# Kernel optimization log

Hardware: AMD Instinct MI355X
Metric: run time of the kernel (lower is better)

## Reference

```python
import jax, jax.numpy as jnp
import numpy as np

B = 128          # batch of codewords
M_CHK = 288      # n_check_nodes
N_VAR = 576      # n_variable_nodes
K_INFO = 288     # n_information_bits
N_ITER = 5
EDGE_P = 0.02    # ~11-12 edges per check row, LDPC-like sparsity


def setup_inputs() -> dict:
    key = jax.random.key(0)
    k1, k2, k3, k4 = jax.random.split(key, 4)
    inputs = jax.random.normal(k1, (B, N_VAR), dtype=jnp.float32)
    # sparse binary parity-check matrix, batched (keras RNN constants carry batch dim)
    H = jax.random.bernoulli(k2, EDGE_P, (B, M_CHK, N_VAR)).astype(jnp.float32)
    sigma2 = 0.5 + 0.5 * jax.random.uniform(k3, (B, 1), dtype=jnp.float32)
    # learned parameters
    input_ponderation = jnp.ones((N_ITER, 1), dtype=jnp.float32)
    out_ponderation = jnp.ones((N_ITER, 1), dtype=jnp.float32)
    skip_ponderation = jnp.ones((1, 1), dtype=jnp.float32)
    # per-edge check-to-variable weights of the neural BP cell
    w_cv = 1.0 + 0.02 * jax.random.normal(k4, (M_CHK, N_VAR), dtype=jnp.float32)
    gate_logit = jnp.asarray(0.0, dtype=jnp.float32)
    return {"inputs": inputs, "H": H, "sigma2": sigma2,
            "input_ponderation": input_ponderation,
            "out_ponderation": out_ponderation,
            "skip_ponderation": skip_ponderation,
            "w_cv": w_cv, "gate_logit": gate_logit}


def _decode(inputs, H, sigma2, input_ponderation, out_ponderation,
            skip_ponderation, w_cv, gate_logit):
    llrs = -4.0 * inputs / sigma2                                    # [B, n]
    # trainable=True path: normalize by mean |llr|
    norm_llrs = llrs / jnp.mean(jnp.abs(llrs), axis=-1, keepdims=True)
    # tile over iterations and apply input ponderation -> [B, T, n]
    x = norm_llrs[:, None, :] * input_ponderation

    mask = H                                                         # [B, m, n]
    gate = jax.nn.sigmoid(gate_logit)

    def cell(Mstate, x_t):
        # variable-to-check extrinsic messages on edges
        S = jnp.sum(Mstate, axis=1, keepdims=True)                   # [B, 1, n]
        V = (x_t[:, None, :] + S - Mstate) * mask                    # [B, m, n]
        # tanh-product check-node update (product excluding self via divide)
        t = jnp.tanh(0.5 * jnp.clip(V, -15.0, 15.0))
        t_edge = jnp.where(mask > 0, t, 1.0)
        P = jnp.prod(t_edge, axis=-1, keepdims=True)                 # [B, m, 1]
        t_safe = jnp.where(jnp.abs(t_edge) < 1e-7,
                           jnp.where(t_edge >= 0, 1e-7, -1e-7), t_edge)
        r = jnp.clip(P / t_safe, -1.0 + 1e-6, 1.0 - 1e-6)
        M_new = 2.0 * jnp.arctanh(r) * w_cv * mask                   # weighted c2v
        # gated (damped) state update
        M_out = gate * M_new + (1.0 - gate) * Mstate
        posterior = x_t + jnp.sum(M_out, axis=1)                     # [B, n]
        return M_out, posterior

    M0 = jnp.zeros_like(H)
    xs = jnp.swapaxes(x, 0, 1)                                       # [T, B, n]
    _, posts = jax.lax.scan(cell, M0, xs)
    outputs = jnp.swapaxes(posts, 0, 1)                              # [B, T, n]

    # post-normalization per iteration, weighted pooling over iterations
    norm_out = outputs / jnp.mean(jnp.abs(outputs), axis=-1, keepdims=True)
    pooled = jnp.mean(out_ponderation * norm_out, axis=-2)           # [B, n]
    out = pooled + skip_ponderation * norm_llrs                      # [1,1] broadcast
    return jax.nn.sigmoid(-out[:, :K_INFO])


def reference(inputs, H, sigma2, input_ponderation, out_ponderation,
              skip_ponderation, w_cv, gate_logit):
    return _decode(inputs, H, sigma2, input_ponderation, out_ponderation,
                   skip_ponderation, w_cv, gate_logit)
```

## Files before the change

### kernel.cpp

```cpp
#include <hip/hip_runtime.h>

#define B_SZ 128
#define MCHK 288
#define NVAR 576
#define KINFO 288
#define NITER 5
#define CAP 40
#define LCAP 3712
#define TPB 1024
#define EPT 4

__device__ __align__(16) unsigned short g_idx[(size_t)B_SZ * MCHK * CAP];
__device__ int g_cnt[B_SZ * MCHK];

__global__ __launch_bounds__(256) void build_edges(const float* __restrict__ H) {
    const int row  = blockIdx.x * 4 + (threadIdx.x >> 6);
    const int lane = threadIdx.x & 63;
    const float* hrow = H + (size_t)row * NVAR;
    const float4* h4  = (const float4*)hrow;
    float4 a  = h4[lane];
    float4 bq = h4[64 + lane];
    float  c  = hrow[512 + lane];
    int cnt = (a.x!=0.f)+(a.y!=0.f)+(a.z!=0.f)+(a.w!=0.f)
            + (bq.x!=0.f)+(bq.y!=0.f)+(bq.z!=0.f)+(bq.w!=0.f) + (c!=0.f);
    int pre = cnt;
    #pragma unroll
    for (int o = 1; o < 64; o <<= 1) {
        int n = __shfl_up(pre, o, 64);
        if (lane >= o) pre += n;
    }
    int p = pre - cnt;
    unsigned short* dst = g_idx + (size_t)row * CAP;
    int base = lane * 4;
    if (a.x!=0.f)  { if (p<CAP) dst[p] = (unsigned short)(base    ); p++; }
    if (a.y!=0.f)  { if (p<CAP) dst[p] = (unsigned short)(base + 1); p++; }
    if (a.z!=0.f)  { if (p<CAP) dst[p] = (unsigned short)(base + 2); p++; }
    if (a.w!=0.f)  { if (p<CAP) dst[p] = (unsigned short)(base + 3); p++; }
    if (bq.x!=0.f) { if (p<CAP) dst[p] = (unsigned short)(256 + base    ); p++; }
    if (bq.y!=0.f) { if (p<CAP) dst[p] = (unsigned short)(256 + base + 1); p++; }
    if (bq.z!=0.f) { if (p<CAP) dst[p] = (unsigned short)(256 + base + 2); p++; }
    if (bq.w!=0.f) { if (p<CAP) dst[p] = (unsigned short)(256 + base + 3); p++; }
    if (c!=0.f)    { if (p<CAP) dst[p] = (unsigned short)(512 + lane);     p++; }
    if (lane == 63) g_cnt[row] = (pre > CAP) ? CAP : pre;
}

__global__ __launch_bounds__(TPB) void decode(
    const float* __restrict__ inp,   const float* __restrict__ sigma2,
    const float* __restrict__ ipond, const float* __restrict__ opond,
    const float* __restrict__ skipp, const float* __restrict__ wcv,
    const float* __restrict__ gatel, float* __restrict__ out) {

    __shared__ __align__(16) float MT[(MCHK * CAP) / 2];
    __shared__ unsigned int ev[LCAP];
    __shared__ float xln[NVAR];
    __shared__ float S[NVAR];
    __shared__ float Prow[MCHK];
    __shared__ int   rcnt[MCHK];
    __shared__ int   roff[MCHK];
    __shared__ float red[16];
    __shared__ float redT[NITER][16];
    __shared__ int   wsumI[16];
    __shared__ int   EtotS;

    float* const tld = MT;
    unsigned short* const stage = (unsigned short*)MT;

    const int b    = blockIdx.x;
    const int tid  = threadIdx.x;
    const int wid  = tid >> 6;
    const int lane = tid & 63;

    const float sig  = sigma2[b];
    const float gate = 1.0f / (1.0f + __expf(-gatel[0]));
    const float gbar = 1.0f - gate;
    const float skip = skipp[0];

    float ipl[NITER], opl[NITER];
    #pragma unroll
    for (int t = 0; t < NITER; ++t) { ipl[t] = ipond[t]; opl[t] = opond[t]; }

    float l = 0.0f;
    if (tid < NVAR) l = -4.0f * inp[(size_t)b * NVAR + tid] / sig;
    float al = (tid < NVAR) ? fabsf(l) : 0.0f;
    #pragma unroll
    for (int o = 32; o; o >>= 1) al += __shfl_down(al, o, 64);
    if (lane == 0) red[wid] = al;

    if (tid < MCHK) rcnt[tid] = g_cnt[b * MCHK + tid];
    {
        const uint4* src = (const uint4*)(g_idx + (size_t)b * (MCHK * CAP));
        uint4* dst = (uint4*)stage;
        const int n16 = (MCHK * CAP * 2) / 16;
        #pragma unroll
        for (int i = 0; i < 2; ++i) {
            const int j = tid + i * TPB;
            if (j < n16) dst[j] = src[j];
        }
    }
    __syncthreads();

    int myc = 0, incl = 0;
    if (tid < 320) {
        myc  = (tid < MCHK) ? rcnt[tid] : 0;
        incl = myc;
        #pragma unroll
        for (int o = 1; o < 64; o <<= 1) {
            int n = __shfl_up(incl, o, 64);
            if (lane >= o) incl += n;
        }
        if (lane == 63) wsumI[wid] = incl;
    }
    __syncthreads();
    if (tid < MCHK) {
        int o = incl - myc;
        #pragma unroll
        for (int w = 0; w < 4; ++w) if (w < wid) o += wsumI[w];
        int c = myc;
        if (o >= LCAP)         { o = 0; c = 0; }
        else if (o + c > LCAP) { c = LCAP - o; }
        roff[tid] = o; rcnt[tid] = c;
        const unsigned short* sg = stage + tid * CAP;
        for (int j = 0; j < c; ++j)
            ev[o + j] = ((unsigned)tid << 16) | (unsigned)sg[j];
    }
    if (tid < NVAR) S[tid] = 0.0f;
    if (tid == 0) {
        int e = wsumI[0] + wsumI[1] + wsumI[2] + wsumI[3] + wsumI[4];
        EtotS = (e > LCAP) ? LCAP : e;
    }
    __syncthreads();
    const int E = EtotS;

    {
        float s = 0.0f;
        #pragma unroll
        for (int i = 0; i < 16; ++i) s += red[i];
        const float sc = (float)NVAR / s;
        if (tid < NVAR) xln[tid] = l * sc;
    }
    unsigned evr[EPT]; float wre[EPT], Ml[EPT], tre[EPT];
    #pragma unroll
    for (int k = 0; k < EPT; ++k) {
        evr[k] = 0u; wre[k] = 0.0f; Ml[k] = 0.0f; tre[k] = 0.0f;
        const int e = tid + k * TPB;
        if (e < E) {
            const unsigned pk = ev[e];
            evr[k] = pk;
            wre[k] = wcv[(pk >> 16) * NVAR + (pk & 0xFFFFu)];
        }
    }
    __syncthreads();

    float p[NITER];
    #pragma unroll
    for (int t = 0; t < NITER; ++t) { p[t] = 0.0f; }

    #pragma unroll
    for (int t = 0; t < NITER; ++t) {
        const float pt = ipl[t];

        #pragma unroll
        for (int k = 0; k < EPT; ++k) {
            const int e = tid + k * TPB;
            if (e < E) {
                const int v = (int)(evr[k] & 0xFFFFu);
                float V = fmaf(pt, xln[v], S[v]) - Ml[k];
                V = fminf(15.0f, fmaxf(-15.0f, V));
                float ex = __expf(V);
                float te = (ex - 1.0f) * __builtin_amdgcn_rcpf(ex + 1.0f);
                float x  = 0.5f * V, x2 = x * x;
                float tp = x * fmaf(x2, fmaf(x2, fmaf(x2, -0.05396825f, 0.13333333f),
                                             -0.33333333f), 1.0f);
                const float tv = (fabsf(V) < 0.5f) ? tp : te;
                tre[k] = tv;
                tld[e] = tv;
            }
        }
        __syncthreads();

        if (tid < MCHK) {
            const int c = rcnt[tid], o = roff[tid];
            float P = 1.0f;
            if (c > 0) {
                float cur = tld[o];
                for (int j = 1; j < c; ++j) {
                    const float nx = tld[o + j];
                    P *= cur;
                    cur = nx;
                }
                P *= cur;
            }
            Prow[tid] = P;
        }
        if (tid < NVAR) {
            if (t > 0) p[t - 1] = fmaf(ipl[t - 1], xln[tid], S[tid]);
            S[tid] = 0.0f;
        }
        __syncthreads();

        #pragma unroll
        for (int k = 0; k < EPT; ++k) {
            const int e = tid + k * TPB;
            if (e < E) {
                const unsigned pk = evr[k];
                const int v = (int)(pk & 0xFFFFu);
                const int m = (int)(pk >> 16);
                const float tj = tre[k];
                const float ts = (fabsf(tj) < 1e-7f) ? ((tj >= 0.0f) ? 1e-7f : -1e-7f) : tj;
                float r = Prow[m] * __builtin_amdgcn_rcpf(ts);
                r = fminf(1.0f - 1e-6f, fmaxf(-1.0f + 1e-6f, r));
                const float Mn = __logf((1.0f + r) * __builtin_amdgcn_rcpf(1.0f - r)) * wre[k];
                const float Mo = fmaf(gate, Mn, gbar * Ml[k]);
                Ml[k] = Mo;
                atomicAdd(&S[v], Mo);
            }
        }
        __syncthreads();
    }

    if (tid < NVAR) p[NITER - 1] = fmaf(ipl[NITER - 1], xln[tid], S[tid]);

    #pragma unroll
    for (int t = 0; t < NITER; ++t) {
        float ap = (tid < NVAR) ? fabsf(p[t]) : 0.0f;
        #pragma unroll
        for (int o = 32; o; o >>= 1) ap += __shfl_down(ap, o, 64);
        if (lane == 0) redT[t][wid] = ap;
    }
    __syncthreads();

    if (tid < KINFO) {
        float pooled = 0.0f;
        #pragma unroll
        for (int t = 0; t < NITER; ++t) {
            float s2 = 0.0f;
            #pragma unroll
            for (int i = 0; i < 16; ++i) s2 += redT[t][i];
            pooled += opl[t] * p[t] * ((float)NVAR / s2);
        }
        float o = pooled * (1.0f / NITER) + skip * xln[tid];
        out[(size_t)b * KINFO + tid] = 1.0f / (1.0f + __expf(o));
    }
}

extern "C" void kernel_launch(void* const* d_in, const int* in_sizes, int n_in,
                              void* d_out, int out_size, void* d_ws, size_t ws_size,
                              hipStream_t stream) {
    const float* inp    = (const float*)d_in[0];
    const float* H      = (const float*)d_in[1];
    const float* sigma2 = (const float*)d_in[2];
    const float* ipond  = (const float*)d_in[3];
    const float* opond  = (const float*)d_in[4];
    const float* skipp  = (const float*)d_in[5];
    const float* wcv    = (const float*)d_in[6];
    const float* gatel  = (const float*)d_in[7];
    float* out = (float*)d_out;

    build_edges<<<(B_SZ * MCHK) / 4, 256, 0, stream>>>(H);
    decode<<<B_SZ, TPB, 0, stream>>>(inp, sigma2, ipond, opond, skipp,
                                     wcv, gatel, out);
}
```

Before: 172.7 us.

## Fuse edge-list build and decode into one kernel with a software grid barrier

Merges the separate H-scanning build_edges kernel and the decode kernel into one launch of 256 blocks. All waves first compact H rows into edge index lists, prefetching the next row into registers. A global atomic-counter barrier then waits until every block is done, and only the first 128 blocks run the decode. This removes one kernel launch and the gap between kernels. In exchange, it depends on all 256 blocks of 1024 threads being resident at once; if they are not, the spin barrier deadlocks.

```diff
diff --git a/kernel.cpp b/kernel.cpp
--- a/kernel.cpp
+++ b/kernel.cpp
@@ -9,42 +9,17 @@
 #define LCAP 3712
 #define TPB 1024
 #define EPT 4
-
-__device__ __align__(16) unsigned short g_idx[(size_t)B_SZ * MCHK * CAP];
-__device__ int g_cnt[B_SZ * MCHK];
-
-__global__ __launch_bounds__(256) void build_edges(const float* __restrict__ H) {
-    const int row  = blockIdx.x * 4 + (threadIdx.x >> 6);
-    const int lane = threadIdx.x & 63;
-    const float* hrow = H + (size_t)row * NVAR;
-    const float4* h4  = (const float4*)hrow;
-    float4 a  = h4[lane];
-    float4 bq = h4[64 + lane];
-    float  c  = hrow[512 + lane];
-    int cnt = (a.x!=0.f)+(a.y!=0.f)+(a.z!=0.f)+(a.w!=0.f)
-            + (bq.x!=0.f)+(bq.y!=0.f)+(bq.z!=0.f)+(bq.w!=0.f) + (c!=0.f);
-    int pre = cnt;
-    #pragma unroll
-    for (int o = 1; o < 64; o <<= 1) {
-        int n = __shfl_up(pre, o, 64);
-        if (lane >= o) pre += n;
-    }
-    int p = pre - cnt;
-    unsigned short* dst = g_idx + (size_t)row * CAP;
-    int base = lane * 4;
-    if (a.x!=0.f)  { if (p<CAP) dst[p] = (unsigned short)(base    ); p++; }
-    if (a.y!=0.f)  { if (p<CAP) dst[p] = (unsigned short)(base + 1); p++; }
-    if (a.z!=0.f)  { if (p<CAP) dst[p] = (unsigned short)(base + 2); p++; }
-    if (a.w!=0.f)  { if (p<CAP) dst[p] = (unsigned short)(base + 3); p++; }
-    if (bq.x!=0.f) { if (p<CAP) dst[p] = (unsigned short)(256 + base    ); p++; }
-    if (bq.y!=0.f) { if (p<CAP) dst[p] = (unsigned short)(256 + base + 1); p++; }
-    if (bq.z!=0.f) { if (p<CAP) dst[p] = (unsigned short)(256 + base + 2); p++; }
-    if (bq.w!=0.f) { if (p<CAP) dst[p] = (unsigned short)(256 + base + 3); p++; }
-    if (c!=0.f)    { if (p<CAP) dst[p] = (unsigned short)(512 + lane);     p++; }
-    if (lane == 63) g_cnt[row] = (pre > CAP) ? CAP : pre;
-}
-
-__global__ __launch_bounds__(TPB) void decode(
+#define GRID 256
+#define NROWS (B_SZ * MCHK)
+#define NWAVE (GRID * (TPB / 64))
+#define RPW (NROWS / NWAVE)
+
+__device__ __align__(16) unsigned short g_idx[(size_t)NROWS * CAP];
+__device__ int g_cnt[NROWS];
+__device__ unsigned g_bar;
+
+__global__ __launch_bounds__(TPB, 4) void fused(
+    const float* __restrict__ H,
     const float* __restrict__ inp,   const float* __restrict__ sigma2,
     const float* __restrict__ ipond, const float* __restrict__ opond,
     const float* __restrict__ skipp, const float* __restrict__ wcv,
@@ -70,7 +45,65 @@
     const int wid  = tid >> 6;
     const int lane = tid & 63;
 
-    const float sig  = sigma2[b];
+    float sig = 1.0f, l = 0.0f;
+    if (b < B_SZ) {
+        sig = sigma2[b];
+        if (tid < NVAR) l = -4.0f * inp[(size_t)b * NVAR + tid] / sig;
+    }
+
+    {
+        const int gw = b * 16 + wid;
+        const float* hr0 = H + (size_t)gw * NVAR;
+        float4 a = ((const float4*)hr0)[lane];
+        float4 q = ((const float4*)hr0)[64 + lane];
+        float  c = hr0[512 + lane];
+        #pragma unroll
+        for (int i = 0; i < RPW; ++i) {
+            const int row = gw + i * NWAVE;
+            float4 na = a, nq = q; float nc = c;
+            if (i < RPW - 1) {
+                const float* hn = H + (size_t)(row + NWAVE) * NVAR;
+                na = ((const float4*)hn)[lane];
+                nq = ((const float4*)hn)[64 + lane];
+                nc = hn[512 + lane];
+            }
+            int cnt = (a.x!=0.f)+(a.y!=0.f)+(a.z!=0.f)+(a.w!=0.f)
+                    + (q.x!=0.f)+(q.y!=0.f)+(q.z!=0.f)+(q.w!=0.f) + (c!=0.f);
+            int pre = cnt;
+            #pragma unroll
+            for (int o = 1; o < 64; o <<= 1) {
+                int n = __shfl_up(pre, o, 64);
+                if (lane >= o) pre += n;
+            }
+            int p = pre - cnt;
+            unsigned short* dst = g_idx + (size_t)row * CAP;
+            int base = lane * 4;
+            if (a.x!=0.f) { if (p<CAP) dst[p] = (unsigned short)(base    ); p++; }
+            if (a.y!=0.f) { if (p<CAP) dst[p] = (unsigned short)(base + 1); p++; }
+            if (a.z!=0.f) { if (p<CAP) dst[p] = (unsigned short)(base + 2); p++; }
+            if (a.w!=0.f) { if (p<CAP) dst[p] = (unsigned short)(base + 3); p++; }
+            if (q.x!=0.f) { if (p<CAP) dst[p] = (unsigned short)(256 + base    ); p++; }
+            if (q.y!=0.f) { if (p<CAP) dst[p] = (unsigned short)(256 + base + 1); p++; }
+            if (q.z!=0.f) { if (p<CAP) dst[p] = (unsigned short)(256 + base + 2); p++; }
+            if (q.w!=0.f) { if (p<CAP) dst[p] = (unsigned short)(256 + base + 3); p++; }
+            if (c!=0.f)   { if (p<CAP) dst[p] = (unsigned short)(512 + lane);     p++; }
+            if (lane == 63) g_cnt[row] = (pre > CAP) ? CAP : pre;
+            a = na; q = nq; c = nc;
+        }
+    }
+
+    __syncthreads();
+    if (tid == 0) {
+        __threadfence();
+        unsigned v = atomicAdd(&g_bar, 1u);
+        unsigned target = (v / (unsigned)GRID + 1u) * (unsigned)GRID;
+        while (atomicAdd(&g_bar, 0u) < target)
+            __builtin_amdgcn_s_sleep(2);
+        __threadfence();
+    }
+    __syncthreads();
+    if (b >= B_SZ) return;
+
     const float gate = 1.0f / (1.0f + __expf(-gatel[0]));
     const float gbar = 1.0f - gate;
     const float skip = skipp[0];
@@ -79,8 +112,6 @@
     #pragma unroll
     for (int t = 0; t < NITER; ++t) { ipl[t] = ipond[t]; opl[t] = opond[t]; }
 
-    float l = 0.0f;
-    if (tid < NVAR) l = -4.0f * inp[(size_t)b * NVAR + tid] / sig;
     float al = (tid < NVAR) ? fabsf(l) : 0.0f;
     #pragma unroll
     for (int o = 32; o; o >>= 1) al += __shfl_down(al, o, 64);
@@ -256,7 +287,6 @@
     const float* gatel  = (const float*)d_in[7];
     float* out = (float*)d_out;
 
-    build_edges<<<(B_SZ * MCHK) / 4, 256, 0, stream>>>(H);
-    decode<<<B_SZ, TPB, 0, stream>>>(inp, sigma2, ipond, opond, skipp,
-                                     wcv, gatel, out);
+    fused<<<GRID, TPB, 0, stream>>>(H, inp, sigma2, ipond, opond, skipp,
+                                    wcv, gatel, out);
 }
```

After: 191.7 us. 1.11x slower.
